# Optimization experiments

Measured on AMD Instinct MI355X. Metric: run time of the kernel, lower is better.

Reference implementation:

```python
import jax, jax.numpy as jnp
import numpy as np

B, T, N_EMBD = 1, 512, 768
N_HEAD, N_KV_HEAD = 12, 6
HEAD_DIM = N_EMBD // N_HEAD  # 64


def rms_norm(x, eps=1e-6):
    return x * jax.lax.rsqrt(jnp.mean(x * x, axis=-1, keepdims=True) + eps)


def apply_rotary_emb(x, cos, sin):
    # x: [B, T, H, D]; cos/sin: [T, D//2]
    d2 = x.shape[-1] // 2
    x1, x2 = x[..., :d2], x[..., d2:]
    c = cos[None, :, None, :]
    s = sin[None, :, None, :]
    return jnp.concatenate([x1 * c - x2 * s, x2 * c + x1 * s], axis=-1)


def tropical_dot_product(q, k):
    # q: [B,H,T,D], k: [B,H,S,D] -> max-plus score [B,H,T,S]
    return jnp.max(q[..., :, None, :] + k[..., None, :, :], axis=-1)


def setup_inputs() -> dict:
    key = jax.random.key(0)
    ks = jax.random.split(key, 5)
    x = jax.random.normal(ks[0], (B, T, N_EMBD), dtype=jnp.float32)
    # Real RoPE tables
    half = HEAD_DIM // 2
    inv_freq = 1.0 / (10000.0 ** (np.arange(0, half, dtype=np.float32) / half))
    t = np.arange(T, dtype=np.float32)
    freqs = np.outer(t, inv_freq)  # [T, D//2]
    cos = jnp.asarray(np.cos(freqs), dtype=jnp.float32)
    sin = jnp.asarray(np.sin(freqs), dtype=jnp.float32)
    std = 0.02
    Wq = std * jax.random.normal(ks[1], (N_EMBD, N_HEAD * HEAD_DIM), dtype=jnp.float32)
    Wk = std * jax.random.normal(ks[2], (N_EMBD, N_KV_HEAD * HEAD_DIM), dtype=jnp.float32)
    Wv = std * jax.random.normal(ks[3], (N_EMBD, N_KV_HEAD * HEAD_DIM), dtype=jnp.float32)
    Wproj = std * jax.random.normal(ks[4], (N_EMBD, N_EMBD), dtype=jnp.float32)
    return {"x": x, "cos": cos, "sin": sin, "Wq": Wq, "Wk": Wk, "Wv": Wv, "Wproj": Wproj}


def reference(x, cos, sin, Wq, Wk, Wv, Wproj):
    b, t, c = x.shape
    q = (x @ Wq).reshape(b, t, N_HEAD, HEAD_DIM)
    k = (x @ Wk).reshape(b, t, N_KV_HEAD, HEAD_DIM)
    v = (x @ Wv).reshape(b, t, N_KV_HEAD, HEAD_DIM)
    q = rms_norm(apply_rotary_emb(q, cos, sin))
    k = rms_norm(apply_rotary_emb(k, cos, sin))
    q = jnp.transpose(q, (0, 2, 1, 3))  # [B,H,T,D]
    k = jnp.transpose(k, (0, 2, 1, 3))  # [B,Hkv,T,D]
    v = jnp.transpose(v, (0, 2, 1, 3))
    n_rep = N_HEAD // N_KV_HEAD
    if n_rep > 1:
        k = jnp.repeat(k, n_rep, axis=1)
        v = jnp.repeat(v, n_rep, axis=1)
    scores = tropical_dot_product(q, k)  # [B,H,T,T]
    causal = jnp.tril(jnp.ones((t, t), dtype=jnp.bool_))
    scores = scores + jnp.where(causal, 0.0, -jnp.inf)
    attn = jax.nn.softmax(scores, axis=-1)
    y = jnp.einsum('bhqk,bhkd->bhqd', attn, v)
    y = jnp.transpose(y, (0, 2, 1, 3)).reshape(b, t, c)
    return y @ Wproj
```

## Files before the change

### kernel.cpp

```cpp
#include <hip/hip_runtime.h>
#include <hip/hip_bf16.h>
#include <math.h>

#define TT   512
#define CEMB 768
#define NH   12
#define NKV  6
#define HD   64
#define KVC  (NKV*HD)

typedef short short8 __attribute__((ext_vector_type(8)));
typedef float floatx4 __attribute__((ext_vector_type(4)));

__device__ __forceinline__ unsigned pack_bf16(float lo, float hi){
  __hip_bfloat162 h = __float22bfloat162_rn(make_float2(lo, hi));
  return *reinterpret_cast<unsigned*>(&h);
}
__device__ __forceinline__ unsigned short bf16_rn(float f){
  unsigned u = __float_as_uint(f);
  u += 0x7FFFu + ((u>>16)&1u);
  return (unsigned short)(u>>16);
}
__device__ __forceinline__ float bf16_to_f32(unsigned short u){
  return __uint_as_float(((unsigned)u) << 16);
}

__global__ void __launch_bounds__(256) gemm_qkv_mfma(
    const float* __restrict__ X,
    const float* __restrict__ Wq, const float* __restrict__ Wk, const float* __restrict__ Wv,
    const float* __restrict__ Wp,
    const float* __restrict__ cosb, const float* __restrict__ sinb,
    float* __restrict__ q, float* __restrict__ k, float* __restrict__ v,
    unsigned short* __restrict__ WpF){
  int bx = blockIdx.x;
  if (bx >= 192){
    int t0 = (bx-192)*256 + threadIdx.x;
    for(int g=0; g<8; ++g){
      int u  = g*9216 + t0;
      int kp = u / 192;
      int n4 = (u - kp*192)*4;
      int kk = kp*2;
      float4 w0 = *(const float4*)&Wp[(size_t)kk*CEMB + n4];
      float4 w1 = *(const float4*)&Wp[(size_t)(kk+1)*CEMB + n4];
      int ks = kk>>5, qq = (kk>>3)&3, j = kk&7;
      #pragma unroll
      for(int i=0;i<4;i++){
        int n = n4+i, ct = n>>4, r = n&15;
        *(unsigned*)&WpF[ (((size_t)(ct*24 + ks)*64 + qq*16 + r)<<3) + j ] =
          pack_bf16((&w0.x)[i], (&w1.x)[i]);
      }
    }
    return;
  }
  int mt = bx / 24, nt = bx % 24;
  const float* W; int ldb, bcol;
  if (nt < 12)      { W = Wq; ldb = CEMB; bcol = nt*64; }
  else if (nt < 18) { W = Wk; ldb = KVC;  bcol = (nt-12)*64; }
  else              { W = Wv; ldb = KVC;  bcol = (nt-18)*64; }

  __shared__ __align__(16) unsigned short Al[2][64][40];
  __shared__ __align__(16) unsigned short Bl[2][64][40];

  int tid = threadIdx.x;
  int am  = tid>>2,  akg = (tid&3)*8;
  int bkp = tid>>4,  bn4 = (tid&15)*4;
  int w = tid>>6, lane = tid&63, qq = lane>>4, r = lane&15;

  floatx4 acc[4];
  #pragma unroll
  for(int c=0;c<4;c++) acc[c] = (floatx4){0.f,0.f,0.f,0.f};

  const float* Ap = X + (size_t)(mt*64 + am)*CEMB + akg;
  const float* Bp = W + (size_t)(2*bkp)*ldb + bcol + bn4;

  float4 a00 = *(const float4*)(Ap);
  float4 a01 = *(const float4*)(Ap + 4);
  float4 b00 = *(const float4*)(Bp);
  float4 b01 = *(const float4*)(Bp + ldb);
  float4 a10 = *(const float4*)(Ap + 32);
  float4 a11 = *(const float4*)(Ap + 36);
  float4 b10 = *(const float4*)(Bp + (size_t)32*ldb);
  float4 b11 = *(const float4*)(Bp + (size_t)33*ldb);

  auto step = [&](int k0, float4& A0, float4& A1, float4& B0, float4& B1,
                  int bufc) {
    unsigned p0 = pack_bf16(A0.x,A0.y), p1 = pack_bf16(A0.z,A0.w);
    unsigned p2 = pack_bf16(A1.x,A1.y), p3 = pack_bf16(A1.z,A1.w);
    *(uint4*)&Al[bufc][am][akg] = make_uint4(p0,p1,p2,p3);
    #pragma unroll
    for(int i=0;i<4;i++)
      *(unsigned*)&Bl[bufc][bn4+i][2*bkp] = pack_bf16((&B0.x)[i], (&B1.x)[i]);
    if (k0 + 64 < CEMB){
      A0 = *(const float4*)(Ap + k0+64);
      A1 = *(const float4*)(Ap + k0+68);
      B0 = *(const float4*)(Bp + (size_t)(k0+64)*ldb);
      B1 = *(const float4*)(Bp + (size_t)(k0+65)*ldb);
    }
    __syncthreads();
    short8 af = *(short8*)&Al[bufc][w*16 + r][qq*8];
    #pragma unroll
    for(int c=0;c<4;c++){
      short8 bfr = *(short8*)&Bl[bufc][c*16 + r][qq*8];
      acc[c] = __builtin_amdgcn_mfma_f32_16x16x32_bf16(af, bfr, acc[c], 0,0,0);
    }
  };

  for(int k0=0; k0<CEMB; k0+=64){
    step(k0,    a00,a01,b00,b01, 0);
    step(k0+32, a10,a11,b10,b11, 1);
  }

  #pragma unroll
  for(int reg=0; reg<4; ++reg){
    int t = mt*64 + w*16 + qq*4 + reg;
    if (nt < 18){
      float cs0 = cosb[t*32 + r],      sn0 = sinb[t*32 + r];
      float cs1 = cosb[t*32 + 16 + r], sn1 = sinb[t*32 + 16 + r];
      float x0 = acc[0][reg], x1 = acc[1][reg], x2 = acc[2][reg], x3 = acc[3][reg];
      float n0 = x0*cs0 - x2*sn0;
      float n1 = x1*cs1 - x3*sn1;
      float n2 = x2*cs0 + x0*sn0;
      float n3 = x3*cs1 + x1*sn1;
      float ss = n0*n0 + n1*n1 + n2*n2 + n3*n3;
      ss += __shfl_xor(ss,1); ss += __shfl_xor(ss,2);
      ss += __shfl_xor(ss,4); ss += __shfl_xor(ss,8);
      float sc = rsqrtf(ss*(1.0f/64.0f) + 1e-6f);
      float* dst = (nt < 12) ? (q + (size_t)t*CEMB + nt*64)
                             : (k + (size_t)t*KVC + (nt-12)*64);
      dst[r]    = n0*sc; dst[16+r] = n1*sc;
      dst[32+r] = n2*sc; dst[48+r] = n3*sc;
    } else {
      float* dst = v + (size_t)t*KVC + (nt-18)*64;
      dst[r]    = acc[0][reg]; dst[16+r] = acc[1][reg];
      dst[32+r] = acc[2][reg]; dst[48+r] = acc[3][reg];
    }
  }
}

__global__ void __launch_bounds__(256, 3) attn_tile(const float* __restrict__ qn,
    const float* __restrict__ kn, const float* __restrict__ vr,
    unsigned short* __restrict__ part_acc, float2* __restrict__ part_ml){
  __shared__ float QPsh[64*68];
  __shared__ float Ksh[64*64];
  __shared__ __align__(16) unsigned short VT[64*72];
  __shared__ __align__(16) unsigned short Pl[64*72];

  int bid = blockIdx.x;
  int lin = (bid & 7)*54 + (bid >> 3);
  int h   = lin / 36;
  int idx = lin % 36;
  int qt = 0, rem = idx;
  while (rem > qt){ rem -= (qt+1); ++qt; }
  int ct = rem;
  int t0 = ct*64;

  int kvh  = h >> 1;
  int w    = threadIdx.x >> 6;
  int lane = threadIdx.x & 63;
  int lg   = lane >> 4;
  int lc   = lane & 15;

  #pragma unroll
  for(int sub=0; sub<4; ++sub){
    int rr = w*16 + sub*4 + lg;
    int sw = ((lc ^ (rr>>2)) & 15)*4;
    *(float4*)&QPsh[rr*68 + lc*4] =
      *(const float4*)&qn[(size_t)(qt*64+rr)*CEMB + h*HD + lc*4];
    *(float4*)&Ksh[rr*64 + sw] =
      *(const float4*)&kn[(size_t)(t0+rr)*KVC + kvh*HD + lc*4];
  }
  {
    int kp = threadIdx.x >> 4;
    int n4 = (threadIdx.x & 15)*4;
    #pragma unroll
    for(int half=0; half<2; ++half){
      int kk = (kp + half*16)*2;
      float4 v0 = *(const float4*)&vr[(size_t)(t0+kk  )*KVC + kvh*HD + n4];
      float4 v1 = *(const float4*)&vr[(size_t)(t0+kk+1)*KVC + kvh*HD + n4];
      #pragma unroll
      for(int i=0;i<4;i++)
        *(unsigned*)&VT[(n4+i)*72 + kk] = pack_bf16((&v0.x)[i], (&v1.x)[i]);
    }
  }
  __syncthreads();

  float s[4][4];
  #pragma unroll
  for(int r=0;r<4;r++)
    #pragma unroll
    for(int c=0;c<4;c++) s[r][c] = -INFINITY;

  #pragma unroll 4
  for(int dg=0; dg<16; ++dg){
    float4 k4[4], q4[4];
    int ksw = ((dg ^ lc)&15)*4;
    #pragma unroll
    for(int c=0;c<4;c++)
      k4[c] = *(const float4*)&Ksh[(lc*4+c)*64 + ksw];
    #pragma unroll
    for(int r=0;r<4;r++)
      q4[r] = *(const float4*)&QPsh[(w*16+lg*4+r)*68 + dg*4];
    #pragma unroll
    for(int r=0;r<4;r++)
      #pragma unroll
      for(int c=0;c<4;c++)
        s[r][c] = fmaxf(s[r][c],
                  fmaxf(fmaxf(q4[r].x + k4[c].x, q4[r].y + k4[c].y),
                        fmaxf(q4[r].z + k4[c].z, q4[r].w + k4[c].w)));
  }

  float mrow[4], lrow[4];
  #pragma unroll
  for(int r=0;r<4;r++){
    int i = qt*64 + w*16 + lg*4 + r;
    #pragma unroll
    for(int c=0;c<4;c++)
      if (t0 + lc*4 + c > i) s[r][c] = -INFINITY;
    float mt = fmaxf(fmaxf(s[r][0],s[r][1]), fmaxf(s[r][2],s[r][3]));
    mt = fmaxf(mt, __shfl_xor(mt,1));
    mt = fmaxf(mt, __shfl_xor(mt,2));
    mt = fmaxf(mt, __shfl_xor(mt,4));
    mt = fmaxf(mt, __shfl_xor(mt,8));
    float p0 = __expf(s[r][0]-mt), p1 = __expf(s[r][1]-mt);
    float p2 = __expf(s[r][2]-mt), p3 = __expf(s[r][3]-mt);
    float ps = p0+p1+p2+p3;
    ps += __shfl_xor(ps,1); ps += __shfl_xor(ps,2);
    ps += __shfl_xor(ps,4); ps += __shfl_xor(ps,8);
    mrow[r] = mt; lrow[r] = ps;
    int row = w*16 + lg*4 + r;
    *(unsigned*)&Pl[row*72 + lc*4]     = pack_bf16(p0,p1);
    *(unsigned*)&Pl[row*72 + lc*4 + 2] = pack_bf16(p2,p3);
    if (lc == 0) part_ml[(h*TT + i)*8 + ct] = make_float2(mrow[r], lrow[r]);
  }
  __builtin_amdgcn_wave_barrier();

  {
    int r_ = lane & 15, qq = lane >> 4;
    floatx4 pacc[4];
    #pragma unroll
    for(int c=0;c<4;c++) pacc[c] = (floatx4){0.f,0.f,0.f,0.f};

    short8 af0 = *(const short8*)&Pl[(w*16+r_)*72 + qq*8];
    short8 af1 = *(const short8*)&Pl[(w*16+r_)*72 + 32 + qq*8];
    #pragma unroll
    for(int c=0;c<4;c++){
      short8 b0 = *(const short8*)&VT[(c*16+r_)*72 + qq*8];
      short8 b1 = *(const short8*)&VT[(c*16+r_)*72 + 32 + qq*8];
      pacc[c] = __builtin_amdgcn_mfma_f32_16x16x32_bf16(af0, b0, pacc[c], 0,0,0);
      pacc[c] = __builtin_amdgcn_mfma_f32_16x16x32_bf16(af1, b1, pacc[c], 0,0,0);
    }

    #pragma unroll
    for(int reg=0; reg<4; ++reg){
      int i = qt*64 + w*16 + qq*4 + reg;
      size_t base = (size_t)((h*TT + i)*8 + ct)*64;
      #pragma unroll
      for(int c=0;c<4;c++)
        part_acc[base + c*16 + r_] = bf16_rn(pacc[c][reg]);
    }
  }
}

__global__ void __launch_bounds__(256) attn_reduce(const unsigned short* __restrict__ part_acc,
    const float2* __restrict__ part_ml, unsigned short* __restrict__ yF){
  int wid  = (blockIdx.x * blockDim.x + threadIdx.x) >> 6;
  int lane = threadIdx.x & 63;
  int h = wid >> 9;
  int i = wid & 511;
  int nch = (i >> 6) + 1;
  int base = (h*TT + i)*8;

  float2 mls[8]; float acs[8];
  #pragma unroll
  for(int c=0;c<8;c++){
    mls[c] = part_ml[base + c];
    acs[c] = bf16_to_f32(part_acc[(size_t)(base + c)*64 + lane]);
  }

  float m = -INFINITY, l = 0.f, a = 0.f;
  #pragma unroll
  for(int c=0;c<8;c++){
    if (c < nch){
      float m_new = fmaxf(m, mls[c].x);
      float sa  = __expf(m - m_new);
      float sc_ = __expf(mls[c].x - m_new);
      l = l*sa + mls[c].y*sc_;
      a = a*sa + acs[c]*sc_;
      m = m_new;
    }
  }
  float val = a / l;
  int s = i>>4, rr = i&15;
  int ks = h*2 + (lane>>5), q2 = (lane>>3)&3, j = lane&7;
  yF[ (((size_t)(s*24 + ks)*64 + q2*16 + rr)<<3) + j ] = bf16_rn(val);
}

__global__ void __launch_bounds__(256) gemm_proj_mfma(
    const unsigned short* __restrict__ yF, const unsigned short* __restrict__ WpF,
    float* __restrict__ out){
  int bx = blockIdx.x;
  int mt = bx / 24, ntH = bx % 24;
  int tid = threadIdx.x, w = tid>>6, lane = tid&63, qq = lane>>4, r = lane&15;
  int s = mt*4 + w;

  const short8* Af = (const short8*)yF  + (size_t)s*24*64 + lane;
  const short8* Bf = (const short8*)WpF + lane;

  floatx4 acc[2];
  acc[0] = (floatx4){0.f,0.f,0.f,0.f};
  acc[1] = (floatx4){0.f,0.f,0.f,0.f};

  short8 ar[4]; short8 br[4][2];
  #pragma unroll
  for(int j=0;j<3;++j){
    ar[j] = Af[(size_t)j*64];
    #pragma unroll
    for(int c=0;c<2;c++) br[j][c] = Bf[(size_t)((ntH*2+c)*24 + j)*64];
  }

  #pragma unroll
  for(int ks=0; ks<24; ++ks){
    int cur = ks & 3;
    if (ks + 3 < 24){
      int nx = (ks+3) & 3;
      ar[nx] = Af[(size_t)(ks+3)*64];
      #pragma unroll
      for(int c=0;c<2;c++) br[nx][c] = Bf[(size_t)((ntH*2+c)*24 + ks+3)*64];
    }
    #pragma unroll
    for(int c=0;c<2;c++)
      acc[c] = __builtin_amdgcn_mfma_f32_16x16x32_bf16(ar[cur], br[cur][c], acc[c], 0,0,0);
  }

  #pragma unroll
  for(int reg=0; reg<4; ++reg){
    int t = mt*64 + w*16 + qq*4 + reg;
    float* dst = out + (size_t)t*CEMB + ntH*32;
    #pragma unroll
    for(int c=0;c<2;c++)
      dst[c*16 + r] = acc[c][reg];
  }
}

extern "C" void kernel_launch(void* const* d_in, const int* in_sizes, int n_in,
                              void* d_out, int out_size, void* d_ws, size_t ws_size,
                              hipStream_t stream){
  const float* x    = (const float*)d_in[0];
  const float* cosb = (const float*)d_in[1];
  const float* sinb = (const float*)d_in[2];
  const float* Wq   = (const float*)d_in[3];
  const float* Wk   = (const float*)d_in[4];
  const float* Wv   = (const float*)d_in[5];
  const float* Wp   = (const float*)d_in[6];
  float* out = (float*)d_out;

  float* ws        = (float*)d_ws;
  float* q_raw     = ws;
  float* k_raw     = q_raw + (size_t)TT*CEMB;
  float* v_raw     = k_raw + (size_t)TT*KVC;
  unsigned short* part_acc = (unsigned short*)(v_raw + (size_t)TT*KVC);
  float2* part_ml  = (float2*)(part_acc + (size_t)NH*TT*8*64);
  unsigned short* WpF = (unsigned short*)(part_ml + (size_t)NH*TT*8);
  unsigned short* yF  = WpF + (size_t)48*24*64*8;

  gemm_qkv_mfma <<<dim3(228),   256, 0, stream>>>(x, Wq, Wk, Wv, Wp, cosb, sinb,
                                                  q_raw, k_raw, v_raw, WpF);
  attn_tile     <<<dim3(432),   256, 0, stream>>>(q_raw, k_raw, v_raw, part_acc, part_ml);
  attn_reduce   <<<dim3(NH*TT/4), 256, 0, stream>>>(part_acc, part_ml, yF);
  gemm_proj_mfma<<<dim3(192),   256, 0, stream>>>(yF, WpF, out);
}
```

Measured before the change: 104.8 us.

## Pre-pack X and QKV weights into bf16 MFMA fragments in separate kernel

Adds a pack_frags kernel that converts X, Wq/Wk/Wv and Wproj into bf16 MFMA-fragment layouts ahead of time. The QKV GEMM then loads fragments straight from global memory into registers with a three-deep register prefetch, with no shared-memory staging or __syncthreads. This removes the LDS round trip and the barriers from the GEMM inner loop. In exchange it adds an extra kernel launch and an extra global write and read of the packed operands.

```diff
diff --git a/kernel.cpp b/kernel.cpp
--- a/kernel.cpp
+++ b/kernel.cpp
@@ -25,89 +25,98 @@
   return __uint_as_float(((unsigned)u) << 16);
 }
 
-__global__ void __launch_bounds__(256) gemm_qkv_mfma(
+__global__ void __launch_bounds__(256) pack_frags(
     const float* __restrict__ X,
     const float* __restrict__ Wq, const float* __restrict__ Wk, const float* __restrict__ Wv,
     const float* __restrict__ Wp,
-    const float* __restrict__ cosb, const float* __restrict__ sinb,
-    float* __restrict__ q, float* __restrict__ k, float* __restrict__ v,
+    unsigned short* __restrict__ XF, unsigned short* __restrict__ WF,
     unsigned short* __restrict__ WpF){
   int bx = blockIdx.x;
-  if (bx >= 192){
-    int t0 = (bx-192)*256 + threadIdx.x;
-    for(int g=0; g<8; ++g){
-      int u  = g*9216 + t0;
-      int kp = u / 192;
-      int n4 = (u - kp*192)*4;
-      int kk = kp*2;
-      float4 w0 = *(const float4*)&Wp[(size_t)kk*CEMB + n4];
-      float4 w1 = *(const float4*)&Wp[(size_t)(kk+1)*CEMB + n4];
-      int ks = kk>>5, qq = (kk>>3)&3, j = kk&7;
-      #pragma unroll
-      for(int i=0;i<4;i++){
-        int n = n4+i, ct = n>>4, r = n&15;
-        *(unsigned*)&WpF[ (((size_t)(ct*24 + ks)*64 + qq*16 + r)<<3) + j ] =
-          pack_bf16((&w0.x)[i], (&w1.x)[i]);
-      }
-    }
+  if (bx < 192){
+    int idx = bx*256 + threadIdx.x;
+    int row = idx / 96, kg = idx - row*96;
+    const float* src = X + (size_t)row*CEMB + kg*8;
+    float4 x0 = *(const float4*)src;
+    float4 x1 = *(const float4*)(src+4);
+    int s = row>>4, r = row&15, ks = kg>>2, qq = kg&3;
+    *(uint4*)&XF[ (((size_t)(s*24 + ks)*64 + qq*16 + r)<<3) ] =
+      make_uint4(pack_bf16(x0.x,x0.y), pack_bf16(x0.z,x0.w),
+                 pack_bf16(x1.x,x1.y), pack_bf16(x1.z,x1.w));
     return;
   }
+  if (bx < 768){
+    int idx = (bx-192)*256 + threadIdx.x;
+    int kp = idx / 384, n4g = idx - kp*384;
+    int kk = kp*2, n = n4g*4;
+    const float* W; int ldb, col;
+    if (n < 768)      { W = Wq; ldb = CEMB; col = n; }
+    else if (n < 1152){ W = Wk; ldb = KVC;  col = n-768; }
+    else              { W = Wv; ldb = KVC;  col = n-1152; }
+    float4 w0 = *(const float4*)&W[(size_t)kk*ldb + col];
+    float4 w1 = *(const float4*)&W[(size_t)(kk+1)*ldb + col];
+    int ks = kk>>5, qq = (kk>>3)&3, j = kk&7;
+    #pragma unroll
+    for(int i=0;i<4;i++){
+      int ni = n+i, nt = ni>>6, c = (ni>>4)&3, r = ni&15;
+      *(unsigned*)&WF[ (((size_t)((nt*4+c)*24 + ks)*64 + qq*16 + r)<<3) + j ] =
+        pack_bf16((&w0.x)[i], (&w1.x)[i]);
+    }
+    return;
+  }
+  int t0 = (bx-768)*256 + threadIdx.x;
+  for(int g=0; g<8; ++g){
+    int u  = g*9216 + t0;
+    int kp = u / 192;
+    int n4 = (u - kp*192)*4;
+    int kk = kp*2;
+    float4 w0 = *(const float4*)&Wp[(size_t)kk*CEMB + n4];
+    float4 w1 = *(const float4*)&Wp[(size_t)(kk+1)*CEMB + n4];
+    int ks = kk>>5, qq = (kk>>3)&3, j = kk&7;
+    #pragma unroll
+    for(int i=0;i<4;i++){
+      int n = n4+i, ct = n>>4, r = n&15;
+      *(unsigned*)&WpF[ (((size_t)(ct*24 + ks)*64 + qq*16 + r)<<3) + j ] =
+        pack_bf16((&w0.x)[i], (&w1.x)[i]);
+    }
+  }
+}
+
+__global__ void __launch_bounds__(256) gemm_qkv_mfma(
+    const unsigned short* __restrict__ XF, const unsigned short* __restrict__ WF,
+    const float* __restrict__ cosb, const float* __restrict__ sinb,
+    float* __restrict__ q, float* __restrict__ k, float* __restrict__ v){
+  int bx = blockIdx.x;
   int mt = bx / 24, nt = bx % 24;
-  const float* W; int ldb, bcol;
-  if (nt < 12)      { W = Wq; ldb = CEMB; bcol = nt*64; }
-  else if (nt < 18) { W = Wk; ldb = KVC;  bcol = (nt-12)*64; }
-  else              { W = Wv; ldb = KVC;  bcol = (nt-18)*64; }
-
-  __shared__ __align__(16) unsigned short Al[2][64][40];
-  __shared__ __align__(16) unsigned short Bl[2][64][40];
-
-  int tid = threadIdx.x;
-  int am  = tid>>2,  akg = (tid&3)*8;
-  int bkp = tid>>4,  bn4 = (tid&15)*4;
-  int w = tid>>6, lane = tid&63, qq = lane>>4, r = lane&15;
+  int tid = threadIdx.x, w = tid>>6, lane = tid&63, qq = lane>>4, r = lane&15;
+  int s = mt*4 + w;
+
+  const short8* Af = (const short8*)XF + (size_t)s*24*64 + lane;
+  const short8* Bf = (const short8*)WF + (size_t)nt*4*24*64 + lane;
 
   floatx4 acc[4];
   #pragma unroll
   for(int c=0;c<4;c++) acc[c] = (floatx4){0.f,0.f,0.f,0.f};
 
-  const float* Ap = X + (size_t)(mt*64 + am)*CEMB + akg;
-  const float* Bp = W + (size_t)(2*bkp)*ldb + bcol + bn4;
-
-  float4 a00 = *(const float4*)(Ap);
-  float4 a01 = *(const float4*)(Ap + 4);
-  float4 b00 = *(const float4*)(Bp);
-  float4 b01 = *(const float4*)(Bp + ldb);
-  float4 a10 = *(const float4*)(Ap + 32);
-  float4 a11 = *(const float4*)(Ap + 36);
-  float4 b10 = *(const float4*)(Bp + (size_t)32*ldb);
-  float4 b11 = *(const float4*)(Bp + (size_t)33*ldb);
-
-  auto step = [&](int k0, float4& A0, float4& A1, float4& B0, float4& B1,
-                  int bufc) {
-    unsigned p0 = pack_bf16(A0.x,A0.y), p1 = pack_bf16(A0.z,A0.w);
-    unsigned p2 = pack_bf16(A1.x,A1.y), p3 = pack_bf16(A1.z,A1.w);
-    *(uint4*)&Al[bufc][am][akg] = make_uint4(p0,p1,p2,p3);
-    #pragma unroll
-    for(int i=0;i<4;i++)
-      *(unsigned*)&Bl[bufc][bn4+i][2*bkp] = pack_bf16((&B0.x)[i], (&B1.x)[i]);
-    if (k0 + 64 < CEMB){
-      A0 = *(const float4*)(Ap + k0+64);
-      A1 = *(const float4*)(Ap + k0+68);
-      B0 = *(const float4*)(Bp + (size_t)(k0+64)*ldb);
-      B1 = *(const float4*)(Bp + (size_t)(k0+65)*ldb);
-    }
-    __syncthreads();
-    short8 af = *(short8*)&Al[bufc][w*16 + r][qq*8];
-    #pragma unroll
-    for(int c=0;c<4;c++){
-      short8 bfr = *(short8*)&Bl[bufc][c*16 + r][qq*8];
-      acc[c] = __builtin_amdgcn_mfma_f32_16x16x32_bf16(af, bfr, acc[c], 0,0,0);
-    }
-  };
-
-  for(int k0=0; k0<CEMB; k0+=64){
-    step(k0,    a00,a01,b00,b01, 0);
-    step(k0+32, a10,a11,b10,b11, 1);
+  short8 ar[3]; short8 br[3][4];
+  #pragma unroll
+  for(int p=0;p<2;++p){
+    ar[p] = Af[(size_t)p*64];
+    #pragma unroll
+    for(int c=0;c<4;c++) br[p][c] = Bf[(size_t)(c*24 + p)*64];
+  }
+
+  #pragma unroll
+  for(int ks=0; ks<24; ++ks){
+    int cur = ks % 3;
+    if (ks + 2 < 24){
+      int nx = (ks+2) % 3;
+      ar[nx] = Af[(size_t)(ks+2)*64];
+      #pragma unroll
+      for(int c=0;c<4;c++) br[nx][c] = Bf[(size_t)(c*24 + ks+2)*64];
+    }
+    #pragma unroll
+    for(int c=0;c<4;c++)
+      acc[c] = __builtin_amdgcn_mfma_f32_16x16x32_bf16(ar[cur], br[cur][c], acc[c], 0,0,0);
   }
 
   #pragma unroll
@@ -362,9 +371,12 @@
   float2* part_ml  = (float2*)(part_acc + (size_t)NH*TT*8*64);
   unsigned short* WpF = (unsigned short*)(part_ml + (size_t)NH*TT*8);
   unsigned short* yF  = WpF + (size_t)48*24*64*8;
-
-  gemm_qkv_mfma <<<dim3(228),   256, 0, stream>>>(x, Wq, Wk, Wv, Wp, cosb, sinb,
-                                                  q_raw, k_raw, v_raw, WpF);
+  unsigned short* XF  = yF  + (size_t)32*24*64*8;
+  unsigned short* WF  = XF  + (size_t)32*24*64*8;
+
+  pack_frags    <<<dim3(804),   256, 0, stream>>>(x, Wq, Wk, Wv, Wp, XF, WF, WpF);
+  gemm_qkv_mfma <<<dim3(192),   256, 0, stream>>>(XF, WF, cosb, sinb,
+                                                  q_raw, k_raw, v_raw);
   attn_tile     <<<dim3(432),   256, 0, stream>>>(q_raw, k_raw, v_raw, part_acc, part_ml);
   attn_reduce   <<<dim3(NH*TT/4), 256, 0, stream>>>(part_acc, part_ml, yF);
   gemm_proj_mfma<<<dim3(192),   256, 0, stream>>>(yF, WpF, out);
```

Measured after the change: 115.8 us. 10.4% more time.
